# Optimization experiments

Measured on AMD Instinct MI355X. Metric: run time of the kernel, lower is better.

## Reference

```python
import jax, jax.numpy as jnp
import numpy as np

VIDEO_DIM, TEXT_DIM, ATTN_DIM = 1024, 768, 512
B, S1, S2 = 8, 256, 64


def setup_inputs() -> dict:
    key = jax.random.key(0)
    ks = jax.random.split(key, 10)
    return {
        "video": jax.random.normal(ks[0], (B, S1, VIDEO_DIM), dtype=jnp.float32),
        "text": jax.random.normal(ks[1], (B, S2, TEXT_DIM), dtype=jnp.float32),
        "video_mask": jax.random.randint(ks[2], (B, S1), 0, 2, dtype=jnp.int32),
        "text_mask": jax.random.randint(ks[3], (B, S2), 0, 2, dtype=jnp.int32),
        "w1": jax.random.normal(ks[4], (VIDEO_DIM, ATTN_DIM), dtype=jnp.float32),
        "w2": jax.random.normal(ks[5], (TEXT_DIM, ATTN_DIM), dtype=jnp.float32),
        "w3": jax.random.normal(ks[6], (ATTN_DIM, 1), dtype=jnp.float32),
        "bias": jax.random.normal(ks[7], (ATTN_DIM,), dtype=jnp.float32),
        "w4": jax.random.normal(ks[8], (ATTN_DIM * 4, 500), dtype=jnp.float32),
        "b4": jax.random.normal(ks[9], (500,), dtype=jnp.float32),
    }


def reference(video, text, video_mask, text_mask, w1, w2, w3, bias, w4, b4):
    # NOTE: original torch code calls h.masked_fill(...) (non in-place) and
    # discards the result, so video_mask/text_mask have NO effect. Faithful.
    # Project before broadcasting (mathematically identical to expand-then-matmul).
    h1 = jnp.einsum("bpd,da->bpa", video, w1)   # [b,s1,a]
    h2 = jnp.einsum("bqd,da->bqa", text, w2)    # [b,s2,a]
    # broadcast additive attention: [b,s1,s2,a]
    h = jnp.tanh(h1[:, :, None, :] + h2[:, None, :, :] + bias)
    e = jnp.einsum("bpqa,ao->bpq", h, w3)       # [b,s1,s2] (w3 has out-dim 1)
    # softmax over text dim (dim=2); the expand to attn_dim is uniform, so
    # softmax per-channel equals softmax of the scalar score.
    scores = jax.nn.softmax(e, axis=2)          # [b,s1,s2]
    text_attn = jnp.einsum("bpq,bqa->bpa", scores, h2)  # [b,s1,a]
    hh = h1                                      # video @ w1, same projection
    cont = jnp.concatenate([hh, text_attn, hh * text_attn, hh - text_attn], axis=-1)
    ret = jnp.einsum("bpc,co->bpo", jnp.tanh(cont), w4) + b4
    return ret
```

## Files before the change

### kernel.cpp

```cpp
#include <hip/hip_runtime.h>
#include <hip/hip_bf16.h>
#include <cstddef>

#define MBP   2048
#define MT    512
#define ADIM  512
#define VDIM  1024
#define TDIM  768
#define NOUT  500
#define CDIM  2048

typedef __attribute__((ext_vector_type(8))) short short8;
typedef __attribute__((ext_vector_type(4))) float floatx4;

__device__ __forceinline__ float tanh_fast(float x) {
    float e = __builtin_amdgcn_exp2f(x * 2.88539008177793f);
    float r = __builtin_amdgcn_rcpf(e + 1.0f);
    return __builtin_fmaf(-2.0f, r, 1.0f);
}

__device__ __forceinline__ unsigned short bf16r(float x) {
    union { float f; unsigned int u; } c; c.f = x;
    unsigned int r = (c.u + 0x7fffu + ((c.u >> 16) & 1u)) >> 16;
    return (unsigned short)r;
}
__device__ __forceinline__ float bf2f(unsigned short h) {
    union { unsigned int u; float f; } c; c.u = ((unsigned int)h) << 16;
    return c.f;
}

__device__ __forceinline__ void split8(float4 a, float4 b, uint4& h, uint4& l) {
    float f[8] = {a.x, a.y, a.z, a.w, b.x, b.y, b.z, b.w};
    unsigned int hu[8], lu[8];
    #pragma unroll
    for (int i = 0; i < 8; ++i) {
        unsigned short hh = bf16r(f[i]);
        hu[i] = hh;
        lu[i] = bf16r(f[i] - bf2f(hh));
    }
    h.x = hu[0] | (hu[1] << 16);
    h.y = hu[2] | (hu[3] << 16);
    h.z = hu[4] | (hu[5] << 16);
    h.w = hu[6] | (hu[7] << 16);
    l.x = lu[0] | (lu[1] << 16);
    l.y = lu[2] | (lu[3] << 16);
    l.z = lu[4] | (lu[5] << 16);
    l.w = lu[6] | (lu[7] << 16);
}

__device__ __forceinline__ void split8s(const float* p, short8& hh, short8& ll) {
    float4 a = *(const float4*)p, b = *(const float4*)(p + 4);
    uint4 h, l; split8(a, b, h, l);
    hh = *(short8*)&h; ll = *(short8*)&l;
}

__device__ __forceinline__ void transp_split_body(
    float (*tile)[33], const float* __restrict__ src,
    unsigned short* __restrict__ hi, unsigned short* __restrict__ lo,
    int R, int C, int bx, int by)
{
    const int tx = threadIdx.x & 31, ty = threadIdx.x >> 5;
    const int r0 = bx * 32, c0 = by * 32;
    #pragma unroll
    for (int i = 0; i < 4; ++i) {
        int r = r0 + ty + i * 8, c = c0 + tx;
        if (r < R && c < C) tile[ty + i * 8][tx] = src[(size_t)r * C + c];
    }
    __syncthreads();
    #pragma unroll
    for (int i = 0; i < 4; ++i) {
        int c = c0 + ty + i * 8, r = r0 + tx;
        if (c < C && r < R) {
            float v = tile[tx][ty + i * 8];
            unsigned short h = bf16r(v);
            hi[(size_t)c * R + r] = h;
            lo[(size_t)c * R + r] = bf16r(v - bf2f(h));
        }
    }
}

__device__ __forceinline__ void transp_single_body(
    float (*tile)[33], const float* __restrict__ src,
    unsigned short* __restrict__ dst, int R, int C, int bx, int by)
{
    const int tx = threadIdx.x & 31, ty = threadIdx.x >> 5;
    const int r0 = bx * 32, c0 = by * 32;
    #pragma unroll
    for (int i = 0; i < 4; ++i) {
        int r = r0 + ty + i * 8, c = c0 + tx;
        if (r < R && c < C) tile[ty + i * 8][tx] = src[(size_t)r * C + c];
    }
    __syncthreads();
    #pragma unroll
    for (int i = 0; i < 4; ++i) {
        int c = c0 + ty + i * 8, r = r0 + tx;
        if (c < C && r < R) dst[(size_t)c * R + r] = bf16r(tile[tx][ty + i * 8]);
    }
}

__global__ __launch_bounds__(256) void prep(
    const float* __restrict__ w1, const float* __restrict__ w2,
    const float* __restrict__ w4,
    unsigned short* __restrict__ w1t_h, unsigned short* __restrict__ w1t_l,
    unsigned short* __restrict__ w2t_h, unsigned short* __restrict__ w2t_l,
    unsigned short* __restrict__ w4t)
{
    __shared__ float tile[32][33];
    const int bid = blockIdx.x;
    if (bid < 512) {
        transp_split_body(tile, w1, w1t_h, w1t_l, VDIM, ADIM, bid & 31, bid >> 5);
    } else if (bid < 896) {
        int idx = bid - 512;
        transp_split_body(tile, w2, w2t_h, w2t_l, TDIM, ADIM, idx % 24, idx / 24);
    } else {
        int idx = bid - 896;
        transp_single_body(tile, w4, w4t, CDIM, NOUT, idx >> 4, idx & 15);
    }
}

#define LP 40

__global__ __launch_bounds__(256) void gemm3_both(
    const float* __restrict__ video, const float* __restrict__ text,
    const unsigned short* __restrict__ w1t_h, const unsigned short* __restrict__ w1t_l,
    const unsigned short* __restrict__ w2t_h, const unsigned short* __restrict__ w2t_l,
    float* __restrict__ h1p, float* __restrict__ h2,
    unsigned short* __restrict__ h2t_h, unsigned short* __restrict__ h2t_l)
{
    __shared__ __align__(16) unsigned short Ahs[2][64 * LP];
    __shared__ __align__(16) unsigned short Als[2][64 * LP];
    __shared__ __align__(16) unsigned short Bhs[2][64 * LP];
    __shared__ __align__(16) unsigned short Bls[2][64 * LP];

    const int bx = blockIdx.x;
    const bool isH2 = (bx >= 64);
    const float* Afp; const unsigned short *Bh, *Bl;
    float* C;
    int Kfull, kbase, nIter, row0;
    if (!isH2) {
        Afp = video; Bh = w1t_h; Bl = w1t_l;
        Kfull = VDIM; kbase = (bx >> 5) * 512; nIter = 16;
        row0 = (bx & 31) * 64;
        C = h1p + (size_t)(bx >> 5) * MBP * ADIM;
    } else {
        Afp = text; Bh = w2t_h; Bl = w2t_l;
        Kfull = TDIM; kbase = 0; nIter = 24;
        row0 = (bx - 64) * 64;
        C = h2;
    }

    const int t = threadIdx.x;
    const int r  = t >> 2;
    const int kc = (t & 3) << 3;
    const int col0 = blockIdx.y * 64;
    const int wave = t >> 6, lane = t & 63;
    const int m15 = lane & 15, q8 = (lane >> 4) << 3;

    const size_t aoff = (size_t)(row0 + r) * Kfull + kbase + kc;
    const size_t boff = (size_t)(col0 + r) * Kfull + kbase + kc;

    floatx4 acc[4] = { {0.f,0.f,0.f,0.f}, {0.f,0.f,0.f,0.f},
                       {0.f,0.f,0.f,0.f}, {0.f,0.f,0.f,0.f} };

    float4 a0 = *(const float4*)(Afp + aoff);
    float4 a1 = *(const float4*)(Afp + aoff + 4);
    uint4 bvh = *(const uint4*)(Bh + boff);
    uint4 bvl = *(const uint4*)(Bl + boff);
    {
        uint4 avh, avl; split8(a0, a1, avh, avl);
        *(uint4*)&Ahs[0][r * LP + kc] = avh;
        *(uint4*)&Als[0][r * LP + kc] = avl;
        *(uint4*)&Bhs[0][r * LP + kc] = bvh;
        *(uint4*)&Bls[0][r * LP + kc] = bvl;
    }

    for (int i = 0; i < nIter; ++i) {
        __syncthreads();
        if (i + 1 < nIter) {
            int k0 = (i + 1) << 5;
            a0 = *(const float4*)(Afp + aoff + k0);
            a1 = *(const float4*)(Afp + aoff + k0 + 4);
            bvh = *(const uint4*)(Bh + boff + k0);
            bvl = *(const uint4*)(Bl + boff + k0);
        }
        const int cur = i & 1;
        short8 afh = *(const short8*)&Ahs[cur][(wave * 16 + m15) * LP + q8];
        short8 afl = *(const short8*)&Als[cur][(wave * 16 + m15) * LP + q8];
        #pragma unroll
        for (int j = 0; j < 4; ++j) {
            short8 bfh = *(const short8*)&Bhs[cur][(j * 16 + m15) * LP + q8];
            short8 bfl = *(const short8*)&Bls[cur][(j * 16 + m15) * LP + q8];
            acc[j] = __builtin_amdgcn_mfma_f32_16x16x32_bf16(afh, bfh, acc[j], 0, 0, 0);
            acc[j] = __builtin_amdgcn_mfma_f32_16x16x32_bf16(afh, bfl, acc[j], 0, 0, 0);
            acc[j] = __builtin_amdgcn_mfma_f32_16x16x32_bf16(afl, bfh, acc[j], 0, 0, 0);
        }
        if (i + 1 < nIter) {
            const int nxt = cur ^ 1;
            uint4 avh, avl; split8(a0, a1, avh, avl);
            *(uint4*)&Ahs[nxt][r * LP + kc] = avh;
            *(uint4*)&Als[nxt][r * LP + kc] = avl;
            *(uint4*)&Bhs[nxt][r * LP + kc] = bvh;
            *(uint4*)&Bls[nxt][r * LP + kc] = bvl;
        }
    }

    const int rbase = row0 + wave * 16 + (q8 >> 1);
    #pragma unroll
    for (int j = 0; j < 4; ++j) {
        int col = col0 + j * 16 + m15;
        #pragma unroll
        for (int rr = 0; rr < 4; ++rr) {
            int row = rbase + rr;
            float v = acc[j][rr];
            C[(size_t)row * ADIM + col] = v;
            if (isH2) {
                size_t idx = (size_t)(row >> 6) * (ADIM * 64) + (size_t)col * 64 + (row & 63);
                unsigned short h = bf16r(v);
                h2t_h[idx] = h;
                h2t_l[idx] = bf16r(v - bf2f(h));
            }
        }
    }
}

__global__ __launch_bounds__(256, 2) void attn_scores(
    const float* __restrict__ h1p,
    const float* __restrict__ h2,
    const float* __restrict__ bias,
    const float* __restrict__ w3,
    float* __restrict__ sc)
{
    __shared__ float h2s[64][132];

    const int bp0 = blockIdx.x * 4;
    const int b   = bp0 >> 8;
    const int t   = threadIdx.x, wave = t >> 6, lane = t & 63;
    const int p   = bp0 + wave;
    const float* h2b  = h2 + (size_t)b * 64 * ADIM;
    const float* h1a  = h1p + (size_t)p * ADIM;
    const float* h1b2 = h1p + (size_t)MBP * ADIM + (size_t)p * ADIM;

    float acc[64];
    #pragma unroll
    for (int q = 0; q < 64; ++q) acc[q] = 0.f;

    const int qrow = t >> 2, cch = t & 3;
    #pragma unroll 1
    for (int tile = 0; tile < 4; ++tile) {
        const int a0 = tile * 128;
        __syncthreads();
        #pragma unroll
        for (int j = 0; j < 8; ++j) {
            float4 v = *(const float4*)(h2b + (size_t)qrow * ADIM + a0 + (cch + 4 * j) * 4);
            *(float4*)&h2s[qrow][(cch + 4 * j) * 4] = v;
        }
        __syncthreads();
        const int ag0 = a0 + lane, ag1 = ag0 + 64;
        const float c0  = h1a[ag0] + h1b2[ag0] + bias[ag0];
        const float c1  = h1a[ag1] + h1b2[ag1] + bias[ag1];
        const float w30 = w3[ag0], w31 = w3[ag1];
        const float* hp = &h2s[0][lane];
        #pragma unroll
        for (int q = 0; q < 64; ++q) {
            acc[q] = __builtin_fmaf(tanh_fast(c0 + hp[q * 132]),      w30, acc[q]);
            acc[q] = __builtin_fmaf(tanh_fast(c1 + hp[q * 132 + 64]), w31, acc[q]);
        }
    }
    __syncthreads();

    float* scr = &h2s[0][0] + wave * 2112;
    const int qq = lane & 31, r0 = (lane >> 5) * 32;
    float e = 0.f;

    #pragma unroll
    for (int q = 0; q < 32; ++q) scr[lane * 33 + q] = acc[q];
    {
        float part = 0.f;
        #pragma unroll
        for (int j = 0; j < 32; ++j) part += scr[(r0 + j) * 33 + qq];
        part += __shfl_xor(part, 32, 64);
        if (lane < 32) e = part;
    }
    #pragma unroll
    for (int q = 0; q < 32; ++q) scr[lane * 33 + q] = acc[32 + q];
    {
        float part = 0.f;
        #pragma unroll
        for (int j = 0; j < 32; ++j) part += scr[(r0 + j) * 33 + qq];
        part += __shfl_xor(part, 32, 64);
        if (lane >= 32) e = part;
    }

    float m = e;
    #pragma unroll
    for (int off = 32; off; off >>= 1) m = fmaxf(m, __shfl_xor(m, off, 64));
    float ex = __builtin_amdgcn_exp2f((e - m) * 1.44269504088896f);
    float s = ex;
    #pragma unroll
    for (int off = 32; off; off >>= 1) s += __shfl_xor(s, off, 64);
    sc[(size_t)p * 64 + lane] = ex * __builtin_amdgcn_rcpf(s);
}

__global__ __launch_bounds__(256) void ta_cont(
    const float* __restrict__ sc32,
    const unsigned short* __restrict__ h2t_h,
    const unsigned short* __restrict__ h2t_l,
    const float* __restrict__ h1p,
    unsigned short* __restrict__ tcont)
{
    const int row0 = blockIdx.x * 64;
    const int col0 = blockIdx.y * 64;
    const int b = row0 >> 8;
    const int t = threadIdx.x;
    const int wave = t >> 6, lane = t & 63;
    const int m15 = lane & 15, q8 = (lane >> 4) << 3;

    const float* ap = sc32 + (size_t)(row0 + wave * 16 + m15) * 64;
    short8 af0h, af0l, af1h, af1l;
    split8s(ap + q8, af0h, af0l);
    split8s(ap + q8 + 32, af1h, af1l);
    const size_t bbase = (size_t)b * ADIM * 64;

    floatx4 acc[4];
    #pragma unroll
    for (int j = 0; j < 4; ++j) {
        size_t boff = bbase + (size_t)(col0 + j * 16 + m15) * 64 + q8;
        short8 bf0h = *(const short8*)&h2t_h[boff];
        short8 bf1h = *(const short8*)&h2t_h[boff + 32];
        short8 bf0l = *(const short8*)&h2t_l[boff];
        short8 bf1l = *(const short8*)&h2t_l[boff + 32];
        floatx4 z = {0.f, 0.f, 0.f, 0.f};
        z = __builtin_amdgcn_mfma_f32_16x16x32_bf16(af0h, bf0h, z, 0, 0, 0);
        z = __builtin_amdgcn_mfma_f32_16x16x32_bf16(af0h, bf0l, z, 0, 0, 0);
        z = __builtin_amdgcn_mfma_f32_16x16x32_bf16(af0l, bf0h, z, 0, 0, 0);
        z = __builtin_amdgcn_mfma_f32_16x16x32_bf16(af1h, bf1h, z, 0, 0, 0);
        z = __builtin_amdgcn_mfma_f32_16x16x32_bf16(af1h, bf1l, z, 0, 0, 0);
        acc[j] = __builtin_amdgcn_mfma_f32_16x16x32_bf16(af1l, bf1h, z, 0, 0, 0);
    }

    const float* h1a  = h1p;
    const float* h1b2 = h1p + (size_t)MBP * ADIM;
    const int rbase = row0 + wave * 16 + (q8 >> 1);
    #pragma unroll
    for (int j = 0; j < 4; ++j) {
        int a = col0 + j * 16 + m15;
        #pragma unroll
        for (int rr = 0; rr < 4; ++rr) {
            int row = rbase + rr;
            float ta = acc[j][rr];
            size_t hi = (size_t)row * ADIM + a;
            float hh = h1a[hi] + h1b2[hi];
            unsigned short* o = tcont + (size_t)row * CDIM;
            o[a]            = bf16r(tanh_fast(hh));
            o[ADIM + a]     = bf16r(tanh_fast(ta));
            o[2 * ADIM + a] = bf16r(tanh_fast(hh * ta));
            o[3 * ADIM + a] = bf16r(tanh_fast(hh - ta));
        }
    }
}

__global__ __launch_bounds__(256) void gemm_bf16(
    const unsigned short* __restrict__ A, const unsigned short* __restrict__ Bt,
    float* __restrict__ P)
{
    __shared__ __align__(16) unsigned short As[2][64 * LP];
    __shared__ __align__(16) unsigned short Bs[2][64 * LP];

    const int t = threadIdx.x;
    const int r  = t >> 2;
    const int kc = (t & 3) << 3;
    const int row0 = blockIdx.x * 64, col0 = blockIdx.y * 64;
    const int kbase = blockIdx.z * 512;
    const int wave = t >> 6, lane = t & 63;
    const int m15 = lane & 15, q8 = (lane >> 4) << 3;

    const unsigned short* Ap = A + (size_t)(row0 + r) * CDIM + kbase + kc;
    const int bn = col0 + r;
    const unsigned short* Bp = Bt + (size_t)bn * CDIM + kbase + kc;
    const bool bvalid = (bn < NOUT);

    floatx4 acc[4] = { {0.f,0.f,0.f,0.f}, {0.f,0.f,0.f,0.f},
                       {0.f,0.f,0.f,0.f}, {0.f,0.f,0.f,0.f} };

    uint4 av = *(const uint4*)Ap;
    uint4 bv = {0u,0u,0u,0u};
    if (bvalid) bv = *(const uint4*)Bp;
    *(uint4*)&As[0][r * LP + kc] = av;
    *(uint4*)&Bs[0][r * LP + kc] = bv;

    const int nIter = 16;
    for (int i = 0; i < nIter; ++i) {
        __syncthreads();
        if (i + 1 < nIter) {
            int k0 = (i + 1) << 5;
            av = *(const uint4*)(Ap + k0);
            if (bvalid) bv = *(const uint4*)(Bp + k0);
        }
        const int cur = i & 1;
        short8 af = *(const short8*)&As[cur][(wave * 16 + m15) * LP + q8];
        #pragma unroll
        for (int j = 0; j < 4; ++j) {
            short8 bf = *(const short8*)&Bs[cur][(j * 16 + m15) * LP + q8];
            acc[j] = __builtin_amdgcn_mfma_f32_16x16x32_bf16(af, bf, acc[j], 0, 0, 0);
        }
        if (i + 1 < nIter) {
            const int nxt = cur ^ 1;
            *(uint4*)&As[nxt][r * LP + kc] = av;
            *(uint4*)&Bs[nxt][r * LP + kc] = bv;
        }
    }

    float* Pz = P + (size_t)blockIdx.z * MBP * 512;
    const int rbase = row0 + wave * 16 + (q8 >> 1);
    #pragma unroll
    for (int j = 0; j < 4; ++j) {
        int col = col0 + j * 16 + m15;
        if (col < NOUT) {
            #pragma unroll
            for (int rr = 0; rr < 4; ++rr)
                Pz[(size_t)(rbase + rr) * 512 + col] = acc[j][rr];
        }
    }
}

__global__ __launch_bounds__(256) void reduce_bias(
    const float* __restrict__ P, const float* __restrict__ b4,
    float* __restrict__ out)
{
    int i = blockIdx.x * 256 + threadIdx.x;
    if (i >= MBP * (NOUT / 2)) return;
    int row = i / (NOUT / 2);
    int col = (i - row * (NOUT / 2)) * 2;
    const float* p = P + (size_t)row * 512 + col;
    float2 v = *(const float2*)(b4 + col);
    #pragma unroll
    for (int z = 0; z < 4; ++z) {
        float2 q = *(const float2*)(p + (size_t)z * MBP * 512);
        v.x += q.x; v.y += q.y;
    }
    *(float2*)(out + (size_t)row * NOUT + col) = v;
}

extern "C" void kernel_launch(void* const* d_in, const int* in_sizes, int n_in,
                              void* d_out, int out_size, void* d_ws, size_t ws_size,
                              hipStream_t stream) {
    const float* video = (const float*)d_in[0];
    const float* text  = (const float*)d_in[1];
    const float* w1   = (const float*)d_in[4];
    const float* w2   = (const float*)d_in[5];
    const float* w3   = (const float*)d_in[6];
    const float* bias = (const float*)d_in[7];
    const float* w4   = (const float*)d_in[8];
    const float* b4   = (const float*)d_in[9];
    float* out = (float*)d_out;

    char* ws = (char*)d_ws;
    size_t off = 0;
    unsigned short* w1t_h = (unsigned short*)(ws + off); off += (size_t)ADIM * VDIM * 2;
    unsigned short* w1t_l = (unsigned short*)(ws + off); off += (size_t)ADIM * VDIM * 2;
    unsigned short* w2t_h = (unsigned short*)(ws + off); off += (size_t)ADIM * TDIM * 2;
    unsigned short* w2t_l = (unsigned short*)(ws + off); off += (size_t)ADIM * TDIM * 2;
    unsigned short* w4t   = (unsigned short*)(ws + off); off += (size_t)NOUT * CDIM * 2;
    float*          h1p   = (float*)(ws + off);          off += (size_t)2 * MBP * ADIM * 4;
    float*          h2    = (float*)(ws + off);          off += (size_t)MT * ADIM * 4;
    unsigned short* h2t_h = (unsigned short*)(ws + off); off += (size_t)8 * ADIM * 64 * 2;
    unsigned short* h2t_l = (unsigned short*)(ws + off); off += (size_t)8 * ADIM * 64 * 2;
    float*          sc32  = (float*)(ws + off);          off += (size_t)MBP * 64 * 4;
    unsigned short* tc    = (unsigned short*)(ws + off); off += (size_t)MBP * CDIM * 2;
    float*          gpart = (float*)(ws + off);          off += (size_t)4 * MBP * 512 * 4;

    prep<<<1920, 256, 0, stream>>>(w1, w2, w4, w1t_h, w1t_l, w2t_h, w2t_l, w4t);

    gemm3_both<<<dim3(72, 8), 256, 0, stream>>>(video, text, w1t_h, w1t_l,
                                                w2t_h, w2t_l, h1p, h2, h2t_h, h2t_l);

    attn_scores<<<MBP / 4, 256, 0, stream>>>(h1p, h2, bias, w3, sc32);

    ta_cont<<<dim3(MBP / 64, ADIM / 64), 256, 0, stream>>>(sc32, h2t_h, h2t_l, h1p, tc);

    gemm_bf16<<<dim3(MBP / 64, 8, 4), 256, 0, stream>>>(tc, w4t, gpart);

    reduce_bias<<<(MBP * (NOUT / 2) + 255) / 256, 256, 0, stream>>>(gpart, b4, out);
}
```

Baseline: 160.7 us.

## Enlarge GEMM tiles to 128x128 with 2x2 wave layout and 4x4 MFMA fragments

```diff
diff --git a/kernel.cpp b/kernel.cpp
--- a/kernel.cpp
+++ b/kernel.cpp
@@ -127,51 +127,66 @@
     float* __restrict__ h1p, float* __restrict__ h2,
     unsigned short* __restrict__ h2t_h, unsigned short* __restrict__ h2t_l)
 {
-    __shared__ __align__(16) unsigned short Ahs[2][64 * LP];
-    __shared__ __align__(16) unsigned short Als[2][64 * LP];
-    __shared__ __align__(16) unsigned short Bhs[2][64 * LP];
-    __shared__ __align__(16) unsigned short Bls[2][64 * LP];
+    __shared__ __align__(16) unsigned short Ahs[2][128 * LP];
+    __shared__ __align__(16) unsigned short Als[2][128 * LP];
+    __shared__ __align__(16) unsigned short Bhs[2][128 * LP];
+    __shared__ __align__(16) unsigned short Bls[2][128 * LP];
 
     const int bx = blockIdx.x;
-    const bool isH2 = (bx >= 64);
+    const bool isH2 = (bx >= 128);
     const float* Afp; const unsigned short *Bh, *Bl;
     float* C;
-    int Kfull, kbase, nIter, row0;
+    int Kfull, kbase, nIter, row0, col0;
     if (!isH2) {
+        int idx = bx & 63;
         Afp = video; Bh = w1t_h; Bl = w1t_l;
-        Kfull = VDIM; kbase = (bx >> 5) * 512; nIter = 16;
-        row0 = (bx & 31) * 64;
-        C = h1p + (size_t)(bx >> 5) * MBP * ADIM;
+        Kfull = VDIM; kbase = (bx >> 6) * 512; nIter = 16;
+        row0 = (idx >> 2) << 7; col0 = (idx & 3) << 7;
+        C = h1p + (size_t)(bx >> 6) * MBP * ADIM;
     } else {
+        int idx = bx - 128;
         Afp = text; Bh = w2t_h; Bl = w2t_l;
         Kfull = TDIM; kbase = 0; nIter = 24;
-        row0 = (bx - 64) * 64;
+        row0 = (idx >> 2) << 7; col0 = (idx & 3) << 7;
         C = h2;
     }
 
     const int t = threadIdx.x;
-    const int r  = t >> 2;
-    const int kc = (t & 3) << 3;
-    const int col0 = blockIdx.y * 64;
+    const int arow = t >> 1;
+    const int kc16 = (t & 1) << 4;
     const int wave = t >> 6, lane = t & 63;
+    const int wr = wave >> 1, wc = wave & 1;
     const int m15 = lane & 15, q8 = (lane >> 4) << 3;
 
-    const size_t aoff = (size_t)(row0 + r) * Kfull + kbase + kc;
-    const size_t boff = (size_t)(col0 + r) * Kfull + kbase + kc;
-
-    floatx4 acc[4] = { {0.f,0.f,0.f,0.f}, {0.f,0.f,0.f,0.f},
-                       {0.f,0.f,0.f,0.f}, {0.f,0.f,0.f,0.f} };
+    const size_t aoff = (size_t)(row0 + arow) * Kfull + kbase + kc16;
+    const size_t boff = (size_t)(col0 + arow) * Kfull + kbase + kc16;
+
+    floatx4 acc[4][4];
+    #pragma unroll
+    for (int mi = 0; mi < 4; ++mi)
+        #pragma unroll
+        for (int ni = 0; ni < 4; ++ni)
+            acc[mi][ni] = floatx4{0.f, 0.f, 0.f, 0.f};
 
     float4 a0 = *(const float4*)(Afp + aoff);
     float4 a1 = *(const float4*)(Afp + aoff + 4);
-    uint4 bvh = *(const uint4*)(Bh + boff);
-    uint4 bvl = *(const uint4*)(Bl + boff);
+    float4 a2 = *(const float4*)(Afp + aoff + 8);
+    float4 a3 = *(const float4*)(Afp + aoff + 12);
+    uint4 bh0 = *(const uint4*)(Bh + boff);
+    uint4 bh1 = *(const uint4*)(Bh + boff + 8);
+    uint4 bl0 = *(const uint4*)(Bl + boff);
+    uint4 bl1 = *(const uint4*)(Bl + boff + 8);
     {
-        uint4 avh, avl; split8(a0, a1, avh, avl);
-        *(uint4*)&Ahs[0][r * LP + kc] = avh;
-        *(uint4*)&Als[0][r * LP + kc] = avl;
-        *(uint4*)&Bhs[0][r * LP + kc] = bvh;
-        *(uint4*)&Bls[0][r * LP + kc] = bvl;
+        uint4 h0, l0, h1v, l1v;
+        split8(a0, a1, h0, l0); split8(a2, a3, h1v, l1v);
+        *(uint4*)&Ahs[0][arow * LP + kc16]     = h0;
+        *(uint4*)&Ahs[0][arow * LP + kc16 + 8] = h1v;
+        *(uint4*)&Als[0][arow * LP + kc16]     = l0;
+        *(uint4*)&Als[0][arow * LP + kc16 + 8] = l1v;
+        *(uint4*)&Bhs[0][arow * LP + kc16]     = bh0;
+        *(uint4*)&Bhs[0][arow * LP + kc16 + 8] = bh1;
+        *(uint4*)&Bls[0][arow * LP + kc16]     = bl0;
+        *(uint4*)&Bls[0][arow * LP + kc16 + 8] = bl1;
     }
 
     for (int i = 0; i < nIter; ++i) {
@@ -180,44 +195,65 @@
             int k0 = (i + 1) << 5;
             a0 = *(const float4*)(Afp + aoff + k0);
             a1 = *(const float4*)(Afp + aoff + k0 + 4);
-            bvh = *(const uint4*)(Bh + boff + k0);
-            bvl = *(const uint4*)(Bl + boff + k0);
+            a2 = *(const float4*)(Afp + aoff + k0 + 8);
+            a3 = *(const float4*)(Afp + aoff + k0 + 12);
+            bh0 = *(const uint4*)(Bh + boff + k0);
+            bh1 = *(const uint4*)(Bh + boff + k0 + 8);
+            bl0 = *(const uint4*)(Bl + boff + k0);
+            bl1 = *(const uint4*)(Bl + boff + k0 + 8);
         }
         const int cur = i & 1;
-        short8 afh = *(const short8*)&Ahs[cur][(wave * 16 + m15) * LP + q8];
-        short8 afl = *(const short8*)&Als[cur][(wave * 16 + m15) * LP + q8];
-        #pragma unroll
-        for (int j = 0; j < 4; ++j) {
-            short8 bfh = *(const short8*)&Bhs[cur][(j * 16 + m15) * LP + q8];
-            short8 bfl = *(const short8*)&Bls[cur][(j * 16 + m15) * LP + q8];
-            acc[j] = __builtin_amdgcn_mfma_f32_16x16x32_bf16(afh, bfh, acc[j], 0, 0, 0);
-            acc[j] = __builtin_amdgcn_mfma_f32_16x16x32_bf16(afh, bfl, acc[j], 0, 0, 0);
-            acc[j] = __builtin_amdgcn_mfma_f32_16x16x32_bf16(afl, bfh, acc[j], 0, 0, 0);
+        short8 bfh[4], bfl[4];
+        #pragma unroll
+        for (int ni = 0; ni < 4; ++ni) {
+            int br = (wc << 6) + ni * 16 + m15;
+            bfh[ni] = *(const short8*)&Bhs[cur][br * LP + q8];
+            bfl[ni] = *(const short8*)&Bls[cur][br * LP + q8];
+        }
+        #pragma unroll
+        for (int mi = 0; mi < 4; ++mi) {
+            int ar = (wr << 6) + mi * 16 + m15;
+            short8 afh = *(const short8*)&Ahs[cur][ar * LP + q8];
+            short8 afl = *(const short8*)&Als[cur][ar * LP + q8];
+            #pragma unroll
+            for (int ni = 0; ni < 4; ++ni) {
+                acc[mi][ni] = __builtin_amdgcn_mfma_f32_16x16x32_bf16(afh, bfh[ni], acc[mi][ni], 0, 0, 0);
+                acc[mi][ni] = __builtin_amdgcn_mfma_f32_16x16x32_bf16(afh, bfl[ni], acc[mi][ni], 0, 0, 0);
+                acc[mi][ni] = __builtin_amdgcn_mfma_f32_16x16x32_bf16(afl, bfh[ni], acc[mi][ni], 0, 0, 0);
+            }
         }
         if (i + 1 < nIter) {
             const int nxt = cur ^ 1;
-            uint4 avh, avl; split8(a0, a1, avh, avl);
-            *(uint4*)&Ahs[nxt][r * LP + kc] = avh;
-            *(uint4*)&Als[nxt][r * LP + kc] = avl;
-            *(uint4*)&Bhs[nxt][r * LP + kc] = bvh;
-            *(uint4*)&Bls[nxt][r * LP + kc] = bvl;
-        }
-    }
-
-    const int rbase = row0 + wave * 16 + (q8 >> 1);
-    #pragma unroll
-    for (int j = 0; j < 4; ++j) {
-        int col = col0 + j * 16 + m15;
-        #pragma unroll
-        for (int rr = 0; rr < 4; ++rr) {
-            int row = rbase + rr;
-            float v = acc[j][rr];
-            C[(size_t)row * ADIM + col] = v;
-            if (isH2) {
-                size_t idx = (size_t)(row >> 6) * (ADIM * 64) + (size_t)col * 64 + (row & 63);
-                unsigned short h = bf16r(v);
-                h2t_h[idx] = h;
-                h2t_l[idx] = bf16r(v - bf2f(h));
+            uint4 h0, l0, h1v, l1v;
+            split8(a0, a1, h0, l0); split8(a2, a3, h1v, l1v);
+            *(uint4*)&Ahs[nxt][arow * LP + kc16]     = h0;
+            *(uint4*)&Ahs[nxt][arow * LP + kc16 + 8] = h1v;
+            *(uint4*)&Als[nxt][arow * LP + kc16]     = l0;
+            *(uint4*)&Als[nxt][arow * LP + kc16 + 8] = l1v;
+            *(uint4*)&Bhs[nxt][arow * LP + kc16]     = bh0;
+            *(uint4*)&Bhs[nxt][arow * LP + kc16 + 8] = bh1;
+            *(uint4*)&Bls[nxt][arow * LP + kc16]     = bl0;
+            *(uint4*)&Bls[nxt][arow * LP + kc16 + 8] = bl1;
+        }
+    }
+
+    #pragma unroll
+    for (int mi = 0; mi < 4; ++mi) {
+        const int rbase = row0 + (wr << 6) + mi * 16 + (q8 >> 1);
+        #pragma unroll
+        for (int ni = 0; ni < 4; ++ni) {
+            int col = col0 + (wc << 6) + ni * 16 + m15;
+            #pragma unroll
+            for (int rr = 0; rr < 4; ++rr) {
+                int row = rbase + rr;
+                float v = acc[mi][ni][rr];
+                C[(size_t)row * ADIM + col] = v;
+                if (isH2) {
+                    size_t idx = (size_t)(row >> 6) * (ADIM * 64) + (size_t)col * 64 + (row & 63);
+                    unsigned short h = bf16r(v);
+                    h2t_h[idx] = h;
+                    h2t_l[idx] = bf16r(v - bf2f(h));
+                }
             }
         }
     }
@@ -359,66 +395,88 @@
     }
 }
 
-__global__ __launch_bounds__(256) void gemm_bf16(
+__global__ __launch_bounds__(256) void gemm_out(
     const unsigned short* __restrict__ A, const unsigned short* __restrict__ Bt,
     float* __restrict__ P)
 {
-    __shared__ __align__(16) unsigned short As[2][64 * LP];
-    __shared__ __align__(16) unsigned short Bs[2][64 * LP];
+    __shared__ __align__(16) unsigned short As[2][128 * LP];
+    __shared__ __align__(16) unsigned short Bs[2][128 * LP];
 
     const int t = threadIdx.x;
-    const int r  = t >> 2;
-    const int kc = (t & 3) << 3;
-    const int row0 = blockIdx.x * 64, col0 = blockIdx.y * 64;
-    const int kbase = blockIdx.z * 512;
+    const int arow = t >> 1;
+    const int kc16 = (t & 1) << 4;
+    const int row0 = blockIdx.x << 7, col0 = blockIdx.y << 7;
+    const int kbase = blockIdx.z << 9;
     const int wave = t >> 6, lane = t & 63;
+    const int wr = wave >> 1, wc = wave & 1;
     const int m15 = lane & 15, q8 = (lane >> 4) << 3;
 
-    const unsigned short* Ap = A + (size_t)(row0 + r) * CDIM + kbase + kc;
-    const int bn = col0 + r;
-    const unsigned short* Bp = Bt + (size_t)bn * CDIM + kbase + kc;
+    const unsigned short* Ap = A + (size_t)(row0 + arow) * CDIM + kbase + kc16;
+    const int bn = col0 + arow;
+    const unsigned short* Bp = Bt + (size_t)bn * CDIM + kbase + kc16;
     const bool bvalid = (bn < NOUT);
 
-    floatx4 acc[4] = { {0.f,0.f,0.f,0.f}, {0.f,0.f,0.f,0.f},
-                       {0.f,0.f,0.f,0.f}, {0.f,0.f,0.f,0.f} };
-
-    uint4 av = *(const uint4*)Ap;
-    uint4 bv = {0u,0u,0u,0u};
-    if (bvalid) bv = *(const uint4*)Bp;
-    *(uint4*)&As[0][r * LP + kc] = av;
-    *(uint4*)&Bs[0][r * LP + kc] = bv;
+    floatx4 acc[4][4];
+    #pragma unroll
+    for (int mi = 0; mi < 4; ++mi)
+        #pragma unroll
+        for (int ni = 0; ni < 4; ++ni)
+            acc[mi][ni] = floatx4{0.f, 0.f, 0.f, 0.f};
+
+    uint4 av0 = *(const uint4*)Ap;
+    uint4 av1 = *(const uint4*)(Ap + 8);
+    uint4 bv0 = {0u,0u,0u,0u}, bv1 = {0u,0u,0u,0u};
+    if (bvalid) { bv0 = *(const uint4*)Bp; bv1 = *(const uint4*)(Bp + 8); }
+    *(uint4*)&As[0][arow * LP + kc16]     = av0;
+    *(uint4*)&As[0][arow * LP + kc16 + 8] = av1;
+    *(uint4*)&Bs[0][arow * LP + kc16]     = bv0;
+    *(uint4*)&Bs[0][arow * LP + kc16 + 8] = bv1;
 
     const int nIter = 16;
     for (int i = 0; i < nIter; ++i) {
         __syncthreads();
         if (i + 1 < nIter) {
             int k0 = (i + 1) << 5;
-            av = *(const uint4*)(Ap + k0);
-            if (bvalid) bv = *(const uint4*)(Bp + k0);
+            av0 = *(const uint4*)(Ap + k0);
+            av1 = *(const uint4*)(Ap + k0 + 8);
+            if (bvalid) { bv0 = *(const uint4*)(Bp + k0); bv1 = *(const uint4*)(Bp + k0 + 8); }
         }
         const int cur = i & 1;
-        short8 af = *(const short8*)&As[cur][(wave * 16 + m15) * LP + q8];
-        #pragma unroll
-        for (int j = 0; j < 4; ++j) {
-            short8 bf = *(const short8*)&Bs[cur][(j * 16 + m15) * LP + q8];
-            acc[j] = __builtin_amdgcn_mfma_f32_16x16x32_bf16(af, bf, acc[j], 0, 0, 0);
+        short8 bf[4];
+        #pragma unroll
+        for (int ni = 0; ni < 4; ++ni) {
+            int br = (wc << 6) + ni * 16 + m15;
+            bf[ni] = *(const short8*)&Bs[cur][br * LP + q8];
+        }
+        #pragma unroll
+        for (int mi = 0; mi < 4; ++mi) {
+            int ar = (wr << 6) + mi * 16 + m15;
+            short8 af = *(const short8*)&As[cur][ar * LP + q8];
+            #pragma unroll
+            for (int ni = 0; ni < 4; ++ni)
+                acc[mi][ni] = __builtin_amdgcn_mfma_f32_16x16x32_bf16(af, bf[ni], acc[mi][ni], 0, 0, 0);
         }
         if (i + 1 < nIter) {
             const int nxt = cur ^ 1;
-            *(uint4*)&As[nxt][r * LP + kc] = av;
-            *(uint4*)&Bs[nxt][r * LP + kc] = bv;
+            *(uint4*)&As[nxt][arow * LP + kc16]     = av0;
+            *(uint4*)&As[nxt][arow * LP + kc16 + 8] = av1;
+            *(uint4*)&Bs[nxt][arow * LP + kc16]     = bv0;
+            *(uint4*)&Bs[nxt][arow * LP + kc16 + 8] = bv1;
         }
     }
 
     float* Pz = P + (size_t)blockIdx.z * MBP * 512;
-    const int rbase = row0 + wave * 16 + (q8 >> 1);
-    #pragma unroll
-    for (int j = 0; j < 4; ++j) {
-        int col = col0 + j * 16 + m15;
-        if (col < NOUT) {
-            #pragma unroll
-            for (int rr = 0; rr < 4; ++rr)
-                Pz[(size_t)(rbase + rr) * 512 + col] = acc[j][rr];
+    #pragma unroll
+    for (int mi = 0; mi < 4; ++mi) {
+        const int rbase = row0 + (wr << 6) + mi * 16 + (q8 >> 1);
+        #pragma unroll
+        for (int ni = 0; ni < 4; ++ni) {
+            int col = col0 + (wc << 6) + ni * 16 + m15;
+            if (col < NOUT) {
+                #pragma unroll
+                for (int rr = 0; rr < 4; ++rr)
+                    Pz[(size_t)(rbase + rr) * 512 + col] = acc[mi][ni][rr];
+            }
         }
     }
 }
@@ -471,14 +529,14 @@
 
     prep<<<1920, 256, 0, stream>>>(w1, w2, w4, w1t_h, w1t_l, w2t_h, w2t_l, w4t);
 
-    gemm3_both<<<dim3(72, 8), 256, 0, stream>>>(video, text, w1t_h, w1t_l,
-                                                w2t_h, w2t_l, h1p, h2, h2t_h, h2t_l);
+    gemm3_both<<<144, 256, 0, stream>>>(video, text, w1t_h, w1t_l,
+                                        w2t_h, w2t_l, h1p, h2, h2t_h, h2t_l);
 
     attn_scores<<<MBP / 4, 256, 0, stream>>>(h1p, h2, bias, w3, sc32);
 
     ta_cont<<<dim3(MBP / 64, ADIM / 64), 256, 0, stream>>>(sc32, h2t_h, h2t_l, h1p, tc);
 
-    gemm_bf16<<<dim3(MBP / 64, 8, 4), 256, 0, stream>>>(tc, w4t, gpart);
+    gemm_out<<<dim3(16, 4, 4), 256, 0, stream>>>(tc, w4t, gpart);
 
     reduce_bias<<<(MBP * (NOUT / 2) + 255) / 256, 256, 0, stream>>>(gpart, b4, out);
 }
```

Result: slower. 188.0 us (+17.0%).
